# Performance work log

Hardware: AMD Instinct MI355X
Metric: run time of the kernel (lower is better)

## Reference

```python
import jax, jax.numpy as jnp
import numpy as np

B = 4096
IN_FEATURES = 4096
OUT_FEATURES = 4096
NNZ = 1677722


def setup_inputs() -> dict:
    key = jax.random.key(0)
    k_x, k_v, k_r, k_c, k_b = jax.random.split(key, 5)
    x = jax.random.normal(k_x, (B, IN_FEATURES), dtype=jnp.float32)
    values = jax.random.normal(k_v, (NNZ,), dtype=jnp.float32)
    rows = jax.random.randint(k_r, (NNZ,), 0, OUT_FEATURES, dtype=jnp.int32)
    cols = jax.random.randint(k_c, (NNZ,), 0, IN_FEATURES, dtype=jnp.int32)
    bias = jax.random.normal(k_b, (OUT_FEATURES,), dtype=jnp.float32) * (1.0 / np.sqrt(IN_FEATURES))
    return {"x": x, "values": values, "rows": rows, "cols": cols, "bias": bias}


def reference(x, values, rows, cols, bias):
    # torch.sparse.mm(W, x.T).T + bias  ==  x @ W.T + bias,
    # where W is the [out, in] COO sparse weight.
    # Scatter COO triplets into a dense [out, in] weight (64MB) once,
    # then use a dense GEMM; duplicate indices accumulate, matching COO semantics.
    W = jnp.zeros((OUT_FEATURES, IN_FEATURES), dtype=values.dtype).at[rows, cols].add(values)
    return x @ W.T + bias  # [B, out]
```

## Files before the change

kernel.cpp:

```cpp
#include <hip/hip_runtime.h>
#include <hip/hip_bf16.h>
#include <cstdint>
#include <cstddef>

#define B_DIM 4096
#define IN_F 4096
#define OUT_F 4096
#define NNZ_N 1677722

typedef short short8 __attribute__((ext_vector_type(8)));
typedef float floatx4 __attribute__((ext_vector_type(4)));
typedef unsigned short ushort8 __attribute__((ext_vector_type(8)));

__device__ inline unsigned short f2bf(float f) {
  union { float f; unsigned int u; } v;
  v.f = f;
  unsigned int u = v.u;
  return (unsigned short)((u + 0x7fffu + ((u >> 16) & 1u)) >> 16);
}

#define P1_CHUNK 8192
#define P1_BLOCKS ((NNZ_N + P1_CHUNK - 1) / P1_CHUNK)
#define NBUCK 512
#define CAP 5120
#define CVT_BLOCKS ((B_DIM * IN_F) / 8 / 1024)

__global__ __launch_bounds__(1024) void p1_bucket_cvt(
    const float* __restrict__ vals, const int* __restrict__ rows,
    const int* __restrict__ cols, unsigned int* __restrict__ gcursor,
    unsigned long long* __restrict__ seg, const float* __restrict__ x,
    unsigned short* __restrict__ xb) {
  __shared__ unsigned int cnt[NBUCK];
  __shared__ unsigned int cur[NBUCK];
  const int b = blockIdx.x;
  if (b < P1_BLOCKS) {
    for (int i = threadIdx.x; i < NBUCK; i += 1024) cnt[i] = 0;
    __syncthreads();
    const int base = b * P1_CHUNK;
#pragma unroll
    for (int j = 0; j < P1_CHUNK / 1024; ++j) {
      int idx = base + j * 1024 + threadIdx.x;
      if (idx < NNZ_N) atomicAdd(&cnt[rows[idx] >> 3], 1u);
    }
    __syncthreads();
    for (int i = threadIdx.x; i < NBUCK; i += 1024) {
      int ii = (i + b * 67) & (NBUCK - 1);
      cur[ii] = atomicAdd(&gcursor[ii], cnt[ii]);
    }
    __syncthreads();
#pragma unroll
    for (int j = 0; j < P1_CHUNK / 1024; ++j) {
      int idx = base + j * 1024 + threadIdx.x;
      if (idx < NNZ_N) {
        int r = rows[idx];
        int c = cols[idx];
        float v = vals[idx];
        int bk = r >> 3;
        unsigned int pos = atomicAdd(&cur[bk], 1u);
        if (pos < CAP) {
          union {
            struct { unsigned int k; float v; } s;
            unsigned long long u;
          } e;
          e.s.k = (((unsigned int)(r & 7)) << 12) | (unsigned int)c;
          e.s.v = v;
          seg[(size_t)bk * CAP + pos] = e.u;
        }
      }
    }
  } else {
    size_t i = ((size_t)(b - P1_BLOCKS) * 1024 + threadIdx.x) * 8;
    float4 a = *(const float4*)(x + i);
    float4 f = *(const float4*)(x + i + 4);
    ushort8 o;
    o[0] = f2bf(a.x); o[1] = f2bf(a.y); o[2] = f2bf(a.z); o[3] = f2bf(a.w);
    o[4] = f2bf(f.x); o[5] = f2bf(f.y); o[6] = f2bf(f.z); o[7] = f2bf(f.w);
    *(ushort8*)(xb + i) = o;
  }
}

__global__ __launch_bounds__(1024) void p2_accum(
    const unsigned int* __restrict__ gcursor,
    const unsigned long long* __restrict__ seg,
    unsigned short* __restrict__ wb) {
  __shared__ float img[8 * 4096];
  const int b = blockIdx.x;
  floatx4* img4 = (floatx4*)img;
  for (int i = threadIdx.x; i < 8192; i += 1024) img4[i] = (floatx4)0.0f;
  __syncthreads();
  unsigned int n = gcursor[b];
  if (n > CAP) n = CAP;
  const unsigned long long* s = seg + (size_t)b * CAP;
  for (unsigned int i = threadIdx.x; i < n; i += 1024) {
    unsigned long long e = s[i];
    unsigned int key = (unsigned int)e;
    union { unsigned int u; float f; } v;
    v.u = (unsigned int)(e >> 32);
    atomicAdd(&img[key & 0x7FFF], v.f);
  }
  __syncthreads();
  unsigned short* dst = wb + (size_t)b * 8 * 4096;
  for (int i = threadIdx.x; i < 4096; i += 1024) {
    floatx4 a = img4[i * 2];
    floatx4 f = img4[i * 2 + 1];
    ushort8 o;
    o[0] = f2bf(a[0]); o[1] = f2bf(a[1]); o[2] = f2bf(a[2]); o[3] = f2bf(a[3]);
    o[4] = f2bf(f[0]); o[5] = f2bf(f[1]); o[6] = f2bf(f[2]); o[7] = f2bf(f[3]);
    *(ushort8*)(dst + i * 8) = o;
  }
}

#define NT_K 64

__device__ inline void load_lds16(const unsigned short* g,
                                  const unsigned short* lds_base) {
  __builtin_amdgcn_global_load_lds(
      (const __attribute__((address_space(1))) unsigned int*)g,
      (__attribute__((address_space(3))) unsigned int*)lds_base, 16, 0, 0);
}

#define SA(DST, tt, q)                                              \
  load_lds16(gA + (size_t)(q) * (64 * IN_F) + (size_t)(tt) * 64,    \
             lAst + (DST) + (q) * 4096)
#define SB(DST, tt, q)                                              \
  load_lds16(gB + (size_t)(q) * (64 * IN_F) + (size_t)(tt) * 64,    \
             lBst + (DST) + (q) * 4096)

#define PH_BAR()                                              \
  do {                                                        \
    asm volatile("" ::: "memory");                            \
    __builtin_amdgcn_s_barrier();                             \
    asm volatile("" ::: "memory");                            \
  } while (0)

#define VMW(n) asm volatile("s_waitcnt vmcnt(" #n ")" ::: "memory")

#define DSR(arr, idx) (*(const short8*)&(arr)[idx])

#define MFMA16(AF, M0, M1)                                                     \
  _Pragma("unroll") for (int j = 0; j < 4; ++j) {                              \
    acc[M0][j] = __builtin_amdgcn_mfma_f32_16x16x32_bf16(AF[0], bf[j][0],      \
                                                         acc[M0][j], 0, 0, 0); \
    acc[M0][j] = __builtin_amdgcn_mfma_f32_16x16x32_bf16(AF[1], bf[j][1],      \
                                                         acc[M0][j], 0, 0, 0); \
    acc[M1][j] = __builtin_amdgcn_mfma_f32_16x16x32_bf16(AF[2], bf[j][0],      \
                                                         acc[M1][j], 0, 0, 0); \
    acc[M1][j] = __builtin_amdgcn_mfma_f32_16x16x32_bf16(AF[3], bf[j][1],      \
                                                         acc[M1][j], 0, 0, 0); \
  }

#define TILE(T, BUF, NBUF, DO_S1, DO_S2, DO_VM4, DO_VM0, DO_RA)               \
  do {                                                                        \
          \
    afB[0] = DSR(lA, (BUF) + aqLo + (32 + rr) * 64 + kc0);                    \
    afB[1] = DSR(lA, (BUF) + aqLo + (32 + rr) * 64 + kc1);                    \
    afB[2] = DSR(lA, (BUF) + aqLo + (48 + rr) * 64 + kc0);                    \
    afB[3] = DSR(lA, (BUF) + aqLo + (48 + rr) * 64 + kc1);                    \
    if (DO_S1) { SA(NBUF, (T) + 1, 1); SA(NBUF, (T) + 1, 3); }                \
    PH_BAR();                                                                 \
    __builtin_amdgcn_s_setprio(1);                                            \
    MFMA16(afA, 0, 1);                                                        \
    __builtin_amdgcn_s_setprio(0);                                            \
    PH_BAR();                                                                 \
          \
    afA[0] = DSR(lA, (BUF) + aqHi + rr * 64 + kc0);                           \
    afA[1] = DSR(lA, (BUF) + aqHi + rr * 64 + kc1);                           \
    afA[2] = DSR(lA, (BUF) + aqHi + (16 + rr) * 64 + kc0);                    \
    afA[3] = DSR(lA, (BUF) + aqHi + (16 + rr) * 64 + kc1);                    \
    if (DO_S2) { SB(BUF, (T) + 2, 0); SB(BUF, (T) + 2, 1); }                  \
    PH_BAR();                                                                 \
    __builtin_amdgcn_s_setprio(1);                                            \
    MFMA16(afB, 2, 3);                                                        \
    __builtin_amdgcn_s_setprio(0);                                            \
    PH_BAR();                                                                 \
                                        \
    afB[0] = DSR(lA, (BUF) + aqHi + (32 + rr) * 64 + kc0);                    \
    afB[1] = DSR(lA, (BUF) + aqHi + (32 + rr) * 64 + kc1);                    \
    afB[2] = DSR(lA, (BUF) + aqHi + (48 + rr) * 64 + kc0);                    \
    afB[3] = DSR(lA, (BUF) + aqHi + (48 + rr) * 64 + kc1);                    \
    if (DO_S2) { SB(BUF, (T) + 2, 2); SB(BUF, (T) + 2, 3); }                  \
    PH_BAR();                                                                 \
    __builtin_amdgcn_s_setprio(1);                                            \
    MFMA16(afA, 4, 5);                                                        \
    __builtin_amdgcn_s_setprio(0);                                            \
    if (DO_VM4) VMW(4);                                                       \
    if (DO_VM0) VMW(0);                                                       \
    PH_BAR();                                                                 \
              \
    if (DO_RA) {                                                              \
      afA[0] = DSR(lA, (NBUF) + aqLo + rr * 64 + kc0);                        \
      afA[1] = DSR(lA, (NBUF) + aqLo + rr * 64 + kc1);                        \
      afA[2] = DSR(lA, (NBUF) + aqLo + (16 + rr) * 64 + kc0);                 \
      afA[3] = DSR(lA, (NBUF) + aqLo + (16 + rr) * 64 + kc1);                 \
    }                                                                         \
    if (DO_S2) { SA(BUF, (T) + 2, 0); SA(BUF, (T) + 2, 2); }                  \
    PH_BAR();                                                                 \
    __builtin_amdgcn_s_setprio(1);                                            \
    MFMA16(afB, 6, 7);                                                        \
    __builtin_amdgcn_s_setprio(0);                                            \
    if (DO_RA) {                                                              \
      _Pragma("unroll") for (int j = 0; j < 4; ++j) {                         \
        bf[j][0] = DSR(lB, (NBUF) + bq + (j * 16 + rr) * 64 + kc0);           \
        bf[j][1] = DSR(lB, (NBUF) + bq + (j * 16 + rr) * 64 + kc1);           \
      }                                                                       \
    }                                                                         \
    PH_BAR();                                                                 \
  } while (0)

__global__ __launch_bounds__(512) void gemm_bt_bf16(
    const unsigned short* __restrict__ A, const unsigned short* __restrict__ Bt,
    const float* __restrict__ bias, float* __restrict__ C) {
  __shared__ unsigned short lA[2 * 16384];
  __shared__ unsigned short lB[2 * 16384];

  const int tid = threadIdx.x;
  const int wid = tid >> 6;
  const int lane = tid & 63;
  const int wm = (wid >> 2) * 128;
  const int wn = (wid & 3) * 64;

  int lin = blockIdx.y * 16 + blockIdx.x;
  lin = (lin & 7) * 32 + (lin >> 3);
  const int bm0 = (lin >> 4) * 256;
  const int bn0 = (lin & 15) * 256;

  const int srow = tid >> 3;
  const int scol = ((tid & 7) ^ (srow & 7)) * 8;
  const unsigned short* gA = A + (size_t)(bm0 + srow) * IN_F + scol;
  const unsigned short* gB = Bt + (size_t)(bn0 + srow) * IN_F + scol;
  unsigned short* lAst = lA + wid * 512;
  unsigned short* lBst = lB + wid * 512;

  const int rr = lane & 15;
  const int kq = lane >> 4;
  const int rx = rr & 7;
  const int kc0 = (kq ^ rx) * 8;
  const int kc1 = kc0 ^ 32;
  const int aqLo = (wm >> 6) * 4096;
  const int aqHi = aqLo + 4096;
  const int bq = (wn >> 6) * 4096;

  floatx4 acc[8][4];
#pragma unroll
  for (int i = 0; i < 8; ++i)
#pragma unroll
    for (int j = 0; j < 4; ++j) acc[i][j] = (floatx4)0.0f;

  short8 bf[4][2];
  short8 afA[4], afB[4];

#pragma unroll
  for (int q = 0; q < 4; ++q) SA(0, 0, q);
#pragma unroll
  for (int q = 0; q < 4; ++q) SB(0, 0, q);
#pragma unroll
  for (int q = 0; q < 4; ++q) SB(16384, 1, q);
  SA(16384, 1, 0);
  SA(16384, 1, 2);
  VMW(6);
  PH_BAR();
#pragma unroll
  for (int j = 0; j < 4; ++j) {
    bf[j][0] = DSR(lB, bq + (j * 16 + rr) * 64 + kc0);
    bf[j][1] = DSR(lB, bq + (j * 16 + rr) * 64 + kc1);
  }
  afA[0] = DSR(lA, aqLo + rr * 64 + kc0);
  afA[1] = DSR(lA, aqLo + rr * 64 + kc1);
  afA[2] = DSR(lA, aqLo + (16 + rr) * 64 + kc0);
  afA[3] = DSR(lA, aqLo + (16 + rr) * 64 + kc1);

  for (int t = 0; t < NT_K - 2; t += 2) {
    TILE(t, 0, 16384, 1, 1, 1, 0, 1);
    TILE(t + 1, 16384, 0, 1, 1, 1, 0, 1);
  }
  TILE(NT_K - 2, 0, 16384, 1, 0, 0, 1, 1);
  TILE(NT_K - 1, 16384, 0, 0, 0, 0, 0, 0);

  const int cn = lane & 15;
  const int r0 = (lane >> 4) * 4;
#pragma unroll
  for (int j = 0; j < 4; ++j) {
    const int col = bn0 + wn + j * 16 + cn;
    const float bv = bias[col];
#pragma unroll
    for (int i = 0; i < 8; ++i) {
#pragma unroll
      for (int r = 0; r < 4; ++r) {
        const int row = bm0 + wm + i * 16 + r0 + r;
        C[(size_t)row * OUT_F + col] = acc[i][j][r] + bv;
      }
    }
  }
}

extern "C" void kernel_launch(void* const* d_in, const int* in_sizes, int n_in,
                              void* d_out, int out_size, void* d_ws,
                              size_t ws_size, hipStream_t stream) {
  const float* x = (const float*)d_in[0];
  const float* vals = (const float*)d_in[1];
  const int* rows = (const int*)d_in[2];
  const int* cols = (const int*)d_in[3];
  const float* bias = (const float*)d_in[4];
  float* out = (float*)d_out;

  unsigned int* gcursor = (unsigned int*)d_ws;
  unsigned long long* seg =
      (unsigned long long*)((char*)d_ws + ((size_t)1 << 20));
  unsigned short* wb = (unsigned short*)((char*)d_ws + ((size_t)32 << 20));
  unsigned short* xb = (unsigned short*)((char*)d_ws + ((size_t)64 << 20));

  (void)hipMemsetAsync(gcursor, 0, NBUCK * sizeof(unsigned int), stream);
  p1_bucket_cvt<<<P1_BLOCKS + CVT_BLOCKS, 1024, 0, stream>>>(
      vals, rows, cols, gcursor, seg, x, xb);
  p2_accum<<<NBUCK, 1024, 0, stream>>>(gcursor, seg, wb);

  gemm_bt_bf16<<<dim3(16, 16), 512, 0, stream>>>(xb, wb, bias, out);
}
```

Measured before the change: 289.0 us.

## Stage COO entries in LDS sorted by bucket before coalesced global writes

The bucketing pass now runs a block-local prefix scan over bucket counts and scatters entries into an LDS staging buffer ordered by bucket. It then writes each bucket's run to its global segment contiguously, replacing per-element scattered global stores with mostly coalesced ones. The cost is extra scan barriers and a 64KB LDS buffer per block, which lowers occupancy for both the bucketing and the x-conversion blocks. The packed key now stores the full row instead of only the low 3 bits, so the accumulate kernel's decoding must mask the row correctly.

```diff
diff --git a/kernel.cpp b/kernel.cpp
--- a/kernel.cpp
+++ b/kernel.cpp
@@ -31,45 +31,66 @@
     unsigned long long* __restrict__ seg, const float* __restrict__ x,
     unsigned short* __restrict__ xb) {
   __shared__ unsigned int cnt[NBUCK];
-  __shared__ unsigned int cur[NBUCK];
+  __shared__ unsigned int off[NBUCK];
+  __shared__ unsigned int offx[NBUCK];
+  __shared__ unsigned int cur2[NBUCK];
+  __shared__ unsigned int gbase[NBUCK];
+  __shared__ unsigned long long stage[P1_CHUNK];
+  __shared__ unsigned int total;
   const int b = blockIdx.x;
+  const int tid = threadIdx.x;
   if (b < P1_BLOCKS) {
-    for (int i = threadIdx.x; i < NBUCK; i += 1024) cnt[i] = 0;
+    if (tid < NBUCK) cnt[tid] = 0;
     __syncthreads();
     const int base = b * P1_CHUNK;
 #pragma unroll
     for (int j = 0; j < P1_CHUNK / 1024; ++j) {
-      int idx = base + j * 1024 + threadIdx.x;
+      int idx = base + j * 1024 + tid;
       if (idx < NNZ_N) atomicAdd(&cnt[rows[idx] >> 3], 1u);
     }
     __syncthreads();
-    for (int i = threadIdx.x; i < NBUCK; i += 1024) {
-      int ii = (i + b * 67) & (NBUCK - 1);
-      cur[ii] = atomicAdd(&gcursor[ii], cnt[ii]);
-    }
+    if (tid < NBUCK) off[tid] = cnt[tid];
+    __syncthreads();
+    for (int s = 1; s < NBUCK; s <<= 1) {
+      unsigned int v = 0;
+      if (tid < NBUCK && tid >= s) v = off[tid - s];
+      __syncthreads();
+      if (tid < NBUCK) off[tid] += v;
+      __syncthreads();
+    }
+    if (tid < NBUCK) {
+      unsigned int e = off[tid] - cnt[tid];
+      offx[tid] = e;
+      cur2[tid] = e;
+      gbase[tid] = atomicAdd(&gcursor[tid], cnt[tid]);
+    }
+    if (tid == NBUCK - 1) total = off[NBUCK - 1];
     __syncthreads();
 #pragma unroll
     for (int j = 0; j < P1_CHUNK / 1024; ++j) {
-      int idx = base + j * 1024 + threadIdx.x;
+      int idx = base + j * 1024 + tid;
       if (idx < NNZ_N) {
         int r = rows[idx];
         int c = cols[idx];
-        float v = vals[idx];
+        union { float f; unsigned int u; } v;
+        v.f = vals[idx];
         int bk = r >> 3;
-        unsigned int pos = atomicAdd(&cur[bk], 1u);
-        if (pos < CAP) {
-          union {
-            struct { unsigned int k; float v; } s;
-            unsigned long long u;
-          } e;
-          e.s.k = (((unsigned int)(r & 7)) << 12) | (unsigned int)c;
-          e.s.v = v;
-          seg[(size_t)bk * CAP + pos] = e.u;
-        }
+        unsigned int slot = atomicAdd(&cur2[bk], 1u);
+        unsigned int key = (((unsigned int)r) << 12) | (unsigned int)c;
+        stage[slot] = ((unsigned long long)v.u << 32) | key;
       }
     }
+    __syncthreads();
+    unsigned int tot = total;
+    for (unsigned int k = tid; k < tot; k += 1024) {
+      unsigned long long e = stage[k];
+      unsigned int key = (unsigned int)e;
+      int bk = key >> 15;
+      unsigned int pos = gbase[bk] + (k - offx[bk]);
+      if (pos < CAP) seg[(size_t)bk * CAP + pos] = e;
+    }
   } else {
-    size_t i = ((size_t)(b - P1_BLOCKS) * 1024 + threadIdx.x) * 8;
+    size_t i = ((size_t)(b - P1_BLOCKS) * 1024 + tid) * 8;
     float4 a = *(const float4*)(x + i);
     float4 f = *(const float4*)(x + i + 4);
     ushort8 o;
```

Result: faster. 276.7 us (-4.3%).
